# Kernel optimization log

Measured on AMD Instinct MI355X. Metric: run time of the kernel, lower is better.

The kernel has to match this reference:

```python
import jax, jax.numpy as jnp
import numpy as np

N = 100_000   # nodes
E = 1_600_000 # edges
C = 64        # in = hidden = out channels
H = 8         # heads
D = C // H    # head_dim = 8
R = 4         # relations
L = 2         # layers


def setup_inputs() -> dict:
    key = jax.random.key(0)
    ks = jax.random.split(key, 10)
    sc = 1.0 / np.sqrt(C)  # xavier-ish scale
    return {
        "x": jax.random.normal(ks[0], (N, C), jnp.float32),
        "edge_index": jax.random.randint(ks[1], (2, E), 0, N),
        "edge_type": jax.random.randint(ks[2], (E,), 0, R),
        "W_Q": jax.random.normal(ks[3], (L, R, H, C, D), jnp.float32) * sc,
        "W_K": jax.random.normal(ks[4], (L, R, H, C, D), jnp.float32) * sc,
        "W_V": jax.random.normal(ks[5], (L, R, H, C, D), jnp.float32) * sc,
        "W_concat": jax.random.normal(ks[6], (L, R, H * D, C), jnp.float32) * sc,
        "sem_w": jax.random.normal(ks[7], (L, C), jnp.float32) * sc,
        "sem_b": jnp.zeros((L,), jnp.float32),
        "W_self": jax.random.normal(ks[8], (L, C, C), jnp.float32) * sc,
        "ln_g": jnp.ones((L, C), jnp.float32),
        "ln_b": jnp.zeros((L, C), jnp.float32),
    }


def _layer(x, src, dst, edge_type, WQ, WK, WV, Wcat, sw, sb, Ws, g, b):
    inv_sqrt_d = 1.0 / np.sqrt(D)
    rel_msgs = []
    for r in range(R):  # small fixed relation loop
        mask = (edge_type == r).astype(x.dtype)             # (E,)
        Q = jnp.einsum('nc,hcd->nhd', x, WQ[r])             # (N,H,D)
        K = jnp.einsum('nc,hcd->nhd', x, WK[r])
        V = jnp.einsum('nc,hcd->nhd', x, WV[r])
        # edge-wise QK energy, leaky_relu(0.01), scatter-add into dst node
        energy = jnp.einsum('ehd,ehd->eh', Q[dst], K[src]) * inv_sqrt_d
        energy = jax.nn.leaky_relu(energy)                  # (E,H)
        alpha_n = jax.ops.segment_sum(energy * mask[:, None], dst,
                                      num_segments=N)       # (N,H)
        alpha = jax.nn.softmax(alpha_n, axis=0)             # softmax over nodes
        w = alpha[dst] * mask[:, None]                      # (E,H)
        m = jax.ops.segment_sum(w[:, :, None] * V[src], dst,
                                num_segments=N)             # (N,H,D)
        rel_msgs.append(m.reshape(N, H * D) @ Wcat[r])      # (N,C)
    stacked = jnp.stack(rel_msgs)                           # (R,N,C)
    beta = jax.nn.softmax(stacked @ sw + sb, axis=0)        # (R,N) semantic attn
    agg = jnp.einsum('rn,rnc->nc', beta, stacked)           # (N,C)
    y = x + jax.nn.gelu(x @ Ws + agg, approximate=False)
    mu = y.mean(-1, keepdims=True)
    var = y.var(-1, keepdims=True)
    return (y - mu) / jnp.sqrt(var + 1e-5) * g + b


def reference(x, edge_index, edge_type, W_Q, W_K, W_V, W_concat,
              sem_w, sem_b, W_self, ln_g, ln_b):
    src, dst = edge_index[0], edge_index[1]  # PyG source_to_target: j=row0, i=row1
    for l in range(L):
        x = _layer(x, src, dst, edge_type, W_Q[l], W_K[l], W_V[l], W_concat[l],
                   sem_w[l], sem_b[l], W_self[l], ln_g[l], ln_b[l])
        # inter-layer dropout omitted (inference / eval mode)
    return x
```

## Files before the change

### kernel.cpp

```cpp
#include <hip/hip_runtime.h>
#include <hip/hip_bf16.h>

#define NN 100000
#define EE 1600000
#define RRR 4
#define HHH 8
#define NT 400000
#define NBUCK 12500
#define BCAP 256

typedef unsigned int u32;
typedef unsigned short u16;
typedef unsigned long long u64;
typedef __attribute__((ext_vector_type(8))) short bf16x8;
typedef __attribute__((ext_vector_type(4))) float f32x4;

static constexpr size_t OFF_KV   = 0;
static constexpr size_t OFF_Q    = 25600000;
static constexpr size_t OFF_S    = 76800000;
static constexpr size_t OFF_AL   = 128000000;
static constexpr size_t OFF_PW   = 140800000;
static constexpr size_t OFF_PART = 141100000;
static constexpr size_t OFF_FIN  = 141110000;
static constexpr size_t OFF_BCNT = 141111008;
static constexpr size_t OFF_BST  = 141161008;
static constexpr size_t OFF_ROWP = 141211008;
static constexpr size_t OFF_EDG  = 142812012;

__device__ inline u16 f2bf(float f){
  union { __hip_bfloat16 h; u16 u; } cv; cv.h = __float2bfloat16(f); return cv.u;
}
__device__ inline float bf2f(u16 u){ return __uint_as_float(((u32)u) << 16); }

__global__ __launch_bounds__(256) void k_binit(u32* __restrict__ bcnt){
  int i = blockIdx.x * 256 + threadIdx.x;
  if (i < NBUCK) bcnt[i] = 0u;
}

__global__ __launch_bounds__(256) void k_bucket(const int* __restrict__ src, const int* __restrict__ dst,
                                                const int* __restrict__ typ, u32* __restrict__ bcnt,
                                                u64* __restrict__ bstore){
  for (int e = blockIdx.x * blockDim.x + threadIdx.x; e < EE; e += gridDim.x * blockDim.x){
    int seg = typ[e] * NN + dst[e];
    int b = seg >> 5;
    u32 pos = atomicAdd(&bcnt[b], 1u);
    if (pos < BCAP) bstore[(size_t)b * BCAP + pos] = ((u64)(u32)seg << 32) | (u32)src[e];
  }
}

__global__ __launch_bounds__(1024) void k_bscan(const u32* __restrict__ bcnt, u32* __restrict__ bstart,
                                                u32* __restrict__ rowp){
  __shared__ u32 tmp[1024];
  int t = threadIdx.x;
  const int PER = (NBUCK + 1023) / 1024;
  u32 loc[PER];
  u32 s = 0;
  #pragma unroll
  for (int i = 0; i < PER; i++){
    int idx = t * PER + i;
    u32 v = (idx < NBUCK) ? min(bcnt[idx], (u32)BCAP) : 0u;
    loc[i] = s; s += v;
  }
  tmp[t] = s; __syncthreads();
  for (int off = 1; off < 1024; off <<= 1){
    u32 add = (t >= off) ? tmp[t - off] : 0u; __syncthreads();
    tmp[t] += add; __syncthreads();
  }
  u32 base = tmp[t] - s;
  #pragma unroll
  for (int i = 0; i < PER; i++){
    int idx = t * PER + i;
    if (idx < NBUCK) bstart[idx] = base + loc[i];
  }
  if (t == 0) rowp[NT] = EE;
}

__global__ __launch_bounds__(256) void k_bsort(const u64* __restrict__ bstore, const u32* __restrict__ bcnt,
                                               const u32* __restrict__ bstart, u32* __restrict__ rowp,
                                               u32* __restrict__ edges){
  __shared__ u16 skey[BCAP];
  __shared__ u32 ssrc[BCAP];
  __shared__ u32 off[32], cur[32], excl[32];
  int b = blockIdx.x, t = threadIdx.x;
  u32 cnt = min(bcnt[b], (u32)BCAP);
  u32 base = bstart[b];
  if (t < 32) off[t] = 0u;
  __syncthreads();
  for (u32 i = t; i < cnt; i += 256){
    u64 v = bstore[(size_t)b * BCAP + i];
    skey[i] = (u16)((v >> 32) & 31u);
    ssrc[i] = (u32)v;
    atomicAdd(&off[(v >> 32) & 31u], 1u);
  }
  __syncthreads();
  if (t == 0){
    u32 acc = 0;
    #pragma unroll
    for (int k = 0; k < 32; k++){ u32 c = off[k]; excl[k] = acc; cur[k] = acc; acc += c; }
  }
  __syncthreads();
  if (t < 32){
    int seg = b * 32 + t;
    if (seg < NT) rowp[seg] = base + excl[t];
  }
  __syncthreads();
  for (u32 i = t; i < cnt; i += 256){
    u32 p = atomicAdd(&cur[skey[i]], 1u);
    edges[base + p] = ssrc[i];
  }
}

__global__ __launch_bounds__(256) void k_repackbf(const float* __restrict__ WQ, const float* __restrict__ WK,
                                                  const float* __restrict__ WV, const float* __restrict__ Wcat,
                                                  const float* __restrict__ Wself, u16* __restrict__ pwB){
  int t = blockIdx.x * 256 + threadIdx.x;
  if (t >= 2 * 17 * 4096) return;
  int l = t / (17 * 4096), rem = t % (17 * 4096);
  int mat = rem >> 12, idx = rem & 4095;
  int out = idx >> 6, c = idx & 63;
  float v;
  if (mat < 12){
    int kind = mat >> 2, r = mat & 3;
    int h = out >> 3, d = out & 7;
    const float* Wsrc = (kind == 0) ? WQ : (kind == 1) ? WK : WV;
    v = Wsrc[((((l * RRR + r) * HHH + h) * 64) + c) * 8 + d];
  } else if (mat == 12){
    v = Wself[(l * 64 + c) * 64 + out];
  } else {
    int r = mat - 13;
    v = Wcat[(((l * RRR + r) * 64) + c) * 64 + out];
  }
  pwB[t] = f2bf(v);
}


__global__ __launch_bounds__(256) void k_qkv(const float* __restrict__ x,
                                             const u16* __restrict__ pwQ, const u16* __restrict__ pwK,
                                             const u16* __restrict__ pwV,
                                             u16* __restrict__ Qr, u32* __restrict__ kvp){
  __shared__ u16 xa[64][72];
  __shared__ u16 wt[3][64][72];
  int t = threadIdx.x;
  int n0 = blockIdx.x * 64;
  {
    int row = t >> 2, c0 = (t & 3) * 16;
    int n = n0 + row;
    float4 v0 = {}, v1 = {}, v2 = {}, v3 = {};
    if (n < NN){
      const float4* xp = (const float4*)(x + (size_t)n * 64 + c0);
      v0 = xp[0]; v1 = xp[1]; v2 = xp[2]; v3 = xp[3];
    }
    ushort4* dp = (ushort4*)&xa[row][c0];
    dp[0] = make_ushort4(f2bf(v0.x), f2bf(v0.y), f2bf(v0.z), f2bf(v0.w));
    dp[1] = make_ushort4(f2bf(v1.x), f2bf(v1.y), f2bf(v1.z), f2bf(v1.w));
    dp[2] = make_ushort4(f2bf(v2.x), f2bf(v2.y), f2bf(v2.z), f2bf(v2.w));
    dp[3] = make_ushort4(f2bf(v3.x), f2bf(v3.y), f2bf(v3.z), f2bf(v3.w));
  }
  {
    const u32* p0 = (const u32*)pwQ;
    const u32* p1 = (const u32*)pwK;
    const u32* p2 = (const u32*)pwV;
    for (int idx = t; idx < 3 * 2048; idx += 256){
      int m = idx >> 11, rem = idx & 2047;
      int out = rem >> 5, cc = rem & 31;
      u32 w = (m == 0) ? p0[rem] : (m == 1) ? p1[rem] : p2[rem];
      *(u32*)&wt[m][out][cc * 2] = w;
    }
  }
  __syncthreads();
  int w = t >> 6, lane = t & 63;
  int ra = w * 16 + (lane & 15);
  int kg = (lane >> 4) * 8;
  int cb = lane & 15;
  int rb = (lane >> 4) * 4;
  bf16x8 a0 = *(const bf16x8*)&xa[ra][kg];
  bf16x8 a1 = *(const bf16x8*)&xa[ra][32 + kg];
  f32x4 z = {0.f, 0.f, 0.f, 0.f};
  {
    f32x4 acc[4] = {z, z, z, z};
    #pragma unroll
    for (int t4 = 0; t4 < 4; t4++){
      bf16x8 b0 = *(const bf16x8*)&wt[0][t4 * 16 + cb][kg];
      bf16x8 b1 = *(const bf16x8*)&wt[0][t4 * 16 + cb][32 + kg];
      acc[t4] = __builtin_amdgcn_mfma_f32_16x16x32_bf16(a0, b0, acc[t4], 0, 0, 0);
      acc[t4] = __builtin_amdgcn_mfma_f32_16x16x32_bf16(a1, b1, acc[t4], 0, 0, 0);
    }
    #pragma unroll
    for (int t4 = 0; t4 < 4; t4++){
      #pragma unroll
      for (int i = 0; i < 4; i++){
        int n = n0 + w * 16 + rb + i;
        if (n < NN) Qr[(size_t)n * 64 + t4 * 16 + cb] = f2bf(acc[t4][i]);
      }
    }
  }
  {
    f32x4 ak[4] = {z, z, z, z};
    f32x4 av[4] = {z, z, z, z};
    #pragma unroll
    for (int t4 = 0; t4 < 4; t4++){
      bf16x8 bk0 = *(const bf16x8*)&wt[1][t4 * 16 + cb][kg];
      bf16x8 bk1 = *(const bf16x8*)&wt[1][t4 * 16 + cb][32 + kg];
      bf16x8 bv0 = *(const bf16x8*)&wt[2][t4 * 16 + cb][kg];
      bf16x8 bv1 = *(const bf16x8*)&wt[2][t4 * 16 + cb][32 + kg];
      ak[t4] = __builtin_amdgcn_mfma_f32_16x16x32_bf16(a0, bk0, ak[t4], 0, 0, 0);
      ak[t4] = __builtin_amdgcn_mfma_f32_16x16x32_bf16(a1, bk1, ak[t4], 0, 0, 0);
      av[t4] = __builtin_amdgcn_mfma_f32_16x16x32_bf16(a0, bv0, av[t4], 0, 0, 0);
      av[t4] = __builtin_amdgcn_mfma_f32_16x16x32_bf16(a1, bv1, av[t4], 0, 0, 0);
    }
    #pragma unroll
    for (int t4 = 0; t4 < 4; t4++){
      #pragma unroll
      for (int i = 0; i < 4; i++){
        int n = n0 + w * 16 + rb + i;
        if (n < NN) kvp[(size_t)n * 64 + t4 * 16 + cb] = (u32)f2bf(ak[t4][i]) | ((u32)f2bf(av[t4][i]) << 16);
      }
    }
  }
}

__global__ __launch_bounds__(256) void k_self(const float* __restrict__ x, const u16* __restrict__ pwS,
                                              u16* __restrict__ outb){
  __shared__ u16 xa[64][72];
  __shared__ u16 wt[64][72];
  int t = threadIdx.x;
  int n0 = blockIdx.x * 64;
  {
    int row = t >> 2, c0 = (t & 3) * 16;
    int n = n0 + row;
    float4 v0 = {}, v1 = {}, v2 = {}, v3 = {};
    if (n < NN){
      const float4* xp = (const float4*)(x + (size_t)n * 64 + c0);
      v0 = xp[0]; v1 = xp[1]; v2 = xp[2]; v3 = xp[3];
    }
    ushort4* dp = (ushort4*)&xa[row][c0];
    dp[0] = make_ushort4(f2bf(v0.x), f2bf(v0.y), f2bf(v0.z), f2bf(v0.w));
    dp[1] = make_ushort4(f2bf(v1.x), f2bf(v1.y), f2bf(v1.z), f2bf(v1.w));
    dp[2] = make_ushort4(f2bf(v2.x), f2bf(v2.y), f2bf(v2.z), f2bf(v2.w));
    dp[3] = make_ushort4(f2bf(v3.x), f2bf(v3.y), f2bf(v3.z), f2bf(v3.w));
  }
  {
    const u32* p0 = (const u32*)pwS;
    for (int idx = t; idx < 2048; idx += 256){
      int out = idx >> 5, cc = idx & 31;
      *(u32*)&wt[out][cc * 2] = p0[idx];
    }
  }
  __syncthreads();
  int w = t >> 6, lane = t & 63;
  int ra = w * 16 + (lane & 15);
  int kg = (lane >> 4) * 8;
  int cb = lane & 15;
  int rb = (lane >> 4) * 4;
  bf16x8 a0 = *(const bf16x8*)&xa[ra][kg];
  bf16x8 a1 = *(const bf16x8*)&xa[ra][32 + kg];
  f32x4 z = {0.f, 0.f, 0.f, 0.f};
  f32x4 acc[4] = {z, z, z, z};
  #pragma unroll
  for (int t4 = 0; t4 < 4; t4++){
    bf16x8 b0 = *(const bf16x8*)&wt[t4 * 16 + cb][kg];
    bf16x8 b1 = *(const bf16x8*)&wt[t4 * 16 + cb][32 + kg];
    acc[t4] = __builtin_amdgcn_mfma_f32_16x16x32_bf16(a0, b0, acc[t4], 0, 0, 0);
    acc[t4] = __builtin_amdgcn_mfma_f32_16x16x32_bf16(a1, b1, acc[t4], 0, 0, 0);
  }
  #pragma unroll
  for (int t4 = 0; t4 < 4; t4++){
    #pragma unroll
    for (int i = 0; i < 4; i++){
      int n = n0 + w * 16 + rb + i;
      if (n < NN) outb[(size_t)n * 64 + t4 * 16 + cb] = f2bf(acc[t4][i]);
    }
  }
}

__global__ __launch_bounds__(256) void k_gather(const u32* __restrict__ edges, const u32* __restrict__ rowpR,
                                                const u32* __restrict__ kvp, const u16* __restrict__ Qr,
                                                u16* __restrict__ Sr, float* __restrict__ alphaR){
  int wid = threadIdx.x >> 6, lane = threadIdx.x & 63;
  int n = blockIdx.x * 4 + wid;
  float q = bf2f(Qr[(size_t)n * 64 + lane]);
  u32 beg = rowpR[n], end = rowpR[n + 1];
  float sa = 0.f, aa = 0.f;
  const float inv_sqrt_d = 0.35355339059327373f;
  for (u32 base = beg; base < end; base += 64){
    u32 cnt = (end - base < 64u) ? (end - base) : 64u;
    u32 eidx = (base + (u32)lane < end) ? edges[base + lane] : 0u;
    u32 j = 0;
    for (; j + 4 <= cnt; j += 4){
      int s0 = __shfl((int)eidx, (int)j);
      int s1 = __shfl((int)eidx, (int)j + 1);
      int s2 = __shfl((int)eidx, (int)j + 2);
      int s3 = __shfl((int)eidx, (int)j + 3);
      u32 w0 = kvp[(size_t)s0 * 64 + lane];
      u32 w1 = kvp[(size_t)s1 * 64 + lane];
      u32 w2 = kvp[(size_t)s2 * 64 + lane];
      u32 w3 = kvp[(size_t)s3 * 64 + lane];
      float p0 = q * bf2f((u16)(w0 & 0xFFFFu));
      float p1 = q * bf2f((u16)(w1 & 0xFFFFu));
      float p2 = q * bf2f((u16)(w2 & 0xFFFFu));
      float p3 = q * bf2f((u16)(w3 & 0xFFFFu));
      p0 += __shfl_xor(p0, 1); p1 += __shfl_xor(p1, 1); p2 += __shfl_xor(p2, 1); p3 += __shfl_xor(p3, 1);
      p0 += __shfl_xor(p0, 2); p1 += __shfl_xor(p1, 2); p2 += __shfl_xor(p2, 2); p3 += __shfl_xor(p3, 2);
      p0 += __shfl_xor(p0, 4); p1 += __shfl_xor(p1, 4); p2 += __shfl_xor(p2, 4); p3 += __shfl_xor(p3, 4);
      float e0 = p0 * inv_sqrt_d; e0 = (e0 > 0.f) ? e0 : 0.01f * e0;
      float e1 = p1 * inv_sqrt_d; e1 = (e1 > 0.f) ? e1 : 0.01f * e1;
      float e2 = p2 * inv_sqrt_d; e2 = (e2 > 0.f) ? e2 : 0.01f * e2;
      float e3 = p3 * inv_sqrt_d; e3 = (e3 > 0.f) ? e3 : 0.01f * e3;
      aa += (e0 + e1) + (e2 + e3);
      sa += (bf2f((u16)(w0 >> 16)) + bf2f((u16)(w1 >> 16))) +
            (bf2f((u16)(w2 >> 16)) + bf2f((u16)(w3 >> 16)));
    }
    for (; j < cnt; ++j){
      int s = __shfl((int)eidx, (int)j);
      u32 w = kvp[(size_t)s * 64 + lane];
      float p = q * bf2f((u16)(w & 0xFFFFu));
      p += __shfl_xor(p, 1);
      p += __shfl_xor(p, 2);
      p += __shfl_xor(p, 4);
      float e = p * inv_sqrt_d;
      e = (e > 0.f) ? e : 0.01f * e;
      aa += e;
      sa += bf2f((u16)(w >> 16));
    }
  }
  Sr[(size_t)n * 64 + lane] = f2bf(sa);
  if ((lane & 7) == 0) alphaR[(size_t)n * 8 + (lane >> 3)] = aa;
}

__global__ __launch_bounds__(256) void k_stats1(const float* __restrict__ alpha, float2* __restrict__ part){
  int col = blockIdx.x;
  int r = col >> 3, h = col & 7;
  int chunk = blockIdx.y;
  const int per = (NN + 31) / 32;
  int nbeg = chunk * per;
  int nend = nbeg + per; if (nend > NN) nend = NN;
  int t = threadIdx.x;
  float m = -1e30f, s = 0.f;
  for (int n = nbeg + t; n < nend; n += 256){
    float a = alpha[((size_t)r * NN + n) * 8 + h];
    if (a > m){ s *= expf(m - a); m = a; }
    s += expf(a - m);
  }
  __shared__ float sm[256], ss[256];
  sm[t] = m; ss[t] = s; __syncthreads();
  for (int off = 128; off > 0; off >>= 1){
    if (t < off){
      float m2 = sm[t + off], s2 = ss[t + off];
      float M = fmaxf(sm[t], m2);
      ss[t] = ss[t] * expf(sm[t] - M) + s2 * expf(m2 - M);
      sm[t] = M;
    }
    __syncthreads();
  }
  if (t == 0) part[col * 32 + chunk] = make_float2(sm[0], ss[0]);
}

__global__ void k_stats2(const float2* __restrict__ part, float2* __restrict__ fin){
  int col = threadIdx.x;
  if (col < 32){
    float M = -1e30f, S = 0.f;
    for (int i = 0; i < 32; i++){
      float2 p = part[col * 32 + i];
      float Mn = fmaxf(M, p.x);
      S = S * expf(M - Mn) + p.y * expf(p.x - Mn);
      M = Mn;
    }
    fin[col] = make_float2(M, 1.f / S);
  }
}

__global__ __launch_bounds__(256) void k_msg(const u16* __restrict__ S, const float* __restrict__ alpha,
                                             const float2* __restrict__ fin, const u16* __restrict__ pwCat,
                                             u16* __restrict__ stacked){
  __shared__ u16 xa[64][72];
  __shared__ u16 wt[64][72];
  int r = blockIdx.y;
  int t = threadIdx.x;
  int n0 = blockIdx.x * 64;
  {
    int row = t >> 2, c0 = (t & 3) * 16;
    int n = n0 + row;
    int na = (n < NN) ? n : (NN - 1);
    int h0 = c0 >> 3;
    float2 f0 = fin[r * 8 + h0];
    float2 f1 = fin[r * 8 + h0 + 1];
    float a0 = alpha[((size_t)r * NN + na) * 8 + h0];
    float a1 = alpha[((size_t)r * NN + na) * 8 + h0 + 1];
    float w0 = expf(a0 - f0.x) * f0.y;
    float w1 = expf(a1 - f1.x) * f1.y;
    const u32* sp = (const u32*)(S + ((size_t)r * NN + na) * 64 + c0);
    #pragma unroll
    for (int jj = 0; jj < 8; jj++){
      u32 bts = sp[jj];
      float wm = (jj < 4) ? w0 : w1;
      ushort2 o;
      o.x = f2bf(bf2f((u16)(bts & 0xFFFFu)) * wm);
      o.y = f2bf(bf2f((u16)(bts >> 16)) * wm);
      *(ushort2*)&xa[row][c0 + jj * 2] = o;
    }
  }
  {
    const u32* p0 = (const u32*)(pwCat + (size_t)r * 4096);
    for (int idx = t; idx < 2048; idx += 256){
      int out = idx >> 5, cc = idx & 31;
      *(u32*)&wt[out][cc * 2] = p0[idx];
    }
  }
  __syncthreads();
  int w = t >> 6, lane = t & 63;
  int ra = w * 16 + (lane & 15);
  int kg = (lane >> 4) * 8;
  int cb = lane & 15;
  int rb = (lane >> 4) * 4;
  bf16x8 a0 = *(const bf16x8*)&xa[ra][kg];
  bf16x8 a1 = *(const bf16x8*)&xa[ra][32 + kg];
  f32x4 z = {0.f, 0.f, 0.f, 0.f};
  f32x4 acc[4] = {z, z, z, z};
  #pragma unroll
  for (int t4 = 0; t4 < 4; t4++){
    bf16x8 b0 = *(const bf16x8*)&wt[t4 * 16 + cb][kg];
    bf16x8 b1 = *(const bf16x8*)&wt[t4 * 16 + cb][32 + kg];
    acc[t4] = __builtin_amdgcn_mfma_f32_16x16x32_bf16(a0, b0, acc[t4], 0, 0, 0);
    acc[t4] = __builtin_amdgcn_mfma_f32_16x16x32_bf16(a1, b1, acc[t4], 0, 0, 0);
  }
  #pragma unroll
  for (int t4 = 0; t4 < 4; t4++){
    #pragma unroll
    for (int i = 0; i < 4; i++){
      int n = n0 + w * 16 + rb + i;
      if (n < NN) stacked[((size_t)r * NN + n) * 64 + t4 * 16 + cb] = f2bf(acc[t4][i]);
    }
  }
}

__global__ __launch_bounds__(256) void k_final(const u16* __restrict__ stacked, const u16* __restrict__ selfb,
                                               const float* __restrict__ xin,
                                               const float* __restrict__ semw, const float* __restrict__ semb,
                                               const float* __restrict__ lng, const float* __restrict__ lnb,
                                               float* __restrict__ xout){
  int t = threadIdx.x;
  int wid = t >> 6, lane = t & 63;
  int n = blockIdx.x * 4 + wid;
  float st[4];
  #pragma unroll
  for (int r = 0; r < 4; r++) st[r] = bf2f(stacked[((size_t)r * NN + n) * 64 + lane]);
  float sw = semw[lane];
  float lg[4];
  #pragma unroll
  for (int r = 0; r < 4; r++){
    float p = st[r] * sw;
    #pragma unroll
    for (int o = 1; o < 64; o <<= 1) p += __shfl_xor(p, o);
    lg[r] = p + semb[0];
  }
  float mx = fmaxf(fmaxf(lg[0], lg[1]), fmaxf(lg[2], lg[3]));
  float e0 = expf(lg[0] - mx), e1 = expf(lg[1] - mx), e2 = expf(lg[2] - mx), e3 = expf(lg[3] - mx);
  float inv = 1.f / (e0 + e1 + e2 + e3);
  float agg = (e0 * st[0] + e1 * st[1] + e2 * st[2] + e3 * st[3]) * inv;
  float pre = bf2f(selfb[(size_t)n * 64 + lane]) + agg;
  float ge = 0.5f * pre * (1.f + erff(pre * 0.70710678118654752f));
  float y = xin[(size_t)n * 64 + lane] + ge;
  float mu = y;
  #pragma unroll
  for (int o = 1; o < 64; o <<= 1) mu += __shfl_xor(mu, o);
  mu *= (1.f / 64.f);
  float d = y - mu;
  float vv = d * d;
  #pragma unroll
  for (int o = 1; o < 64; o <<= 1) vv += __shfl_xor(vv, o);
  vv *= (1.f / 64.f);
  xout[(size_t)n * 64 + lane] = d * rsqrtf(vv + 1e-5f) * lng[lane] + lnb[lane];
}

extern "C" void kernel_launch(void* const* d_in, const int* in_sizes, int n_in,
                              void* d_out, int out_size, void* d_ws, size_t ws_size,
                              hipStream_t stream){
  const float* x0    = (const float*)d_in[0];
  const int*   eidx  = (const int*)d_in[1];
  const int*   etyp  = (const int*)d_in[2];
  const float* WQ    = (const float*)d_in[3];
  const float* WK    = (const float*)d_in[4];
  const float* WV    = (const float*)d_in[5];
  const float* Wcat  = (const float*)d_in[6];
  const float* semw  = (const float*)d_in[7];
  const float* semb  = (const float*)d_in[8];
  const float* Wself = (const float*)d_in[9];
  const float* lng   = (const float*)d_in[10];
  const float* lnb   = (const float*)d_in[11];
  float* out = (float*)d_out;
  char* ws = (char*)d_ws;

  const int* srcArr = eidx;
  const int* dstArr = eidx + EE;

  u32*  kvp      = (u32*)(ws + OFF_KV);
  u16*  selfb    = (u16*)(ws + OFF_KV);
  u16*  Qb       = (u16*)(ws + OFF_Q);
  u16*  stackedB = (u16*)(ws + OFF_Q);
  u16*  Sb       = (u16*)(ws + OFF_S);
  u64*  bstore   = (u64*)(ws + OFF_S);
  float* alphaB  = (float*)(ws + OFF_AL);
  u16*  pwB      = (u16*)(ws + OFF_PW);
  float2* part   = (float2*)(ws + OFF_PART);
  float2* fin    = (float2*)(ws + OFF_FIN);
  u32* bcnt   = (u32*)(ws + OFF_BCNT);
  u32* bstart = (u32*)(ws + OFF_BST);
  u32* rowp   = (u32*)(ws + OFF_ROWP);
  u32* edges  = (u32*)(ws + OFF_EDG);

  k_binit<<<(NBUCK + 255) / 256, 256, 0, stream>>>(bcnt);
  k_bucket<<<1024, 256, 0, stream>>>(srcArr, dstArr, etyp, bcnt, bstore);
  k_bscan<<<1, 1024, 0, stream>>>(bcnt, bstart, rowp);
  k_bsort<<<NBUCK, 256, 0, stream>>>(bstore, bcnt, bstart, rowp, edges);
  k_repackbf<<<(2 * 17 * 4096 + 255) / 256, 256, 0, stream>>>(WQ, WK, WV, Wcat, Wself, pwB);

  for (int l = 0; l < 2; l++){
    const float* xcur = (l == 0) ? x0 : out;
    const u16* pwL = pwB + (size_t)l * 17 * 4096;
    for (int r = 0; r < 4; r++){
      k_qkv<<<1563, 256, 0, stream>>>(xcur, pwL + (size_t)r * 4096, pwL + (size_t)(4 + r) * 4096,
                                      pwL + (size_t)(8 + r) * 4096, Qb + (size_t)r * NN * 64, kvp);
      k_gather<<<NN / 4, 256, 0, stream>>>(edges, rowp + (size_t)r * NN, kvp,
                                           Qb + (size_t)r * NN * 64,
                                           Sb + (size_t)r * NN * 64,
                                           alphaB + (size_t)r * NN * 8);
    }
    k_self<<<1563, 256, 0, stream>>>(xcur, pwL + (size_t)12 * 4096, selfb);
    k_stats1<<<dim3(32, 32), 256, 0, stream>>>(alphaB, part);
    k_stats2<<<1, 64, 0, stream>>>(part, fin);
    k_msg<<<dim3(1563, 4), 256, 0, stream>>>(Sb, alphaB, fin, pwL + (size_t)13 * 4096, stackedB);
    k_final<<<NN / 4, 256, 0, stream>>>(stackedB, selfb, xcur,
                                        semw + l * 64, semb + l, lng + l * 64, lnb + l * 64, out);
  }
  (void)in_sizes; (void)n_in; (void)out_size; (void)ws_size;
}
```

Before: 749.7 us.

## Replace atomic bucket CSR build with two-level histogram counting sort

```diff
diff --git a/kernel.cpp b/kernel.cpp
--- a/kernel.cpp
+++ b/kernel.cpp
@@ -6,12 +6,14 @@
 #define RRR 4
 #define HHH 8
 #define NT 400000
-#define NBUCK 12500
-#define BCAP 256
+#define GG 782
+#define SHIFT 9
+#define NBLK 512
+#define CHUNK 3125
+#define BMAX 2560
 
 typedef unsigned int u32;
 typedef unsigned short u16;
-typedef unsigned long long u64;
 typedef __attribute__((ext_vector_type(8))) short bf16x8;
 typedef __attribute__((ext_vector_type(4))) float f32x4;
 
@@ -22,91 +24,111 @@
 static constexpr size_t OFF_PW   = 140800000;
 static constexpr size_t OFF_PART = 141100000;
 static constexpr size_t OFF_FIN  = 141110000;
-static constexpr size_t OFF_BCNT = 141111008;
-static constexpr size_t OFF_BST  = 141161008;
-static constexpr size_t OFF_ROWP = 141211008;
-static constexpr size_t OFF_EDG  = 142812012;
+static constexpr size_t OFF_ROWP = 141365504;
+static constexpr size_t OFF_EDG  = 142965512;
+static constexpr size_t OFF_BSTORE = OFF_S;
+static constexpr size_t OFF_HIST   = OFF_S + 8000000;
+static constexpr size_t OFF_OFFA   = OFF_S + 16000000;
+static constexpr size_t OFF_BASE   = OFF_S + 24000000;
 
 __device__ inline u16 f2bf(float f){
   union { __hip_bfloat16 h; u16 u; } cv; cv.h = __float2bfloat16(f); return cv.u;
 }
 __device__ inline float bf2f(u16 u){ return __uint_as_float(((u32)u) << 16); }
 
-__global__ __launch_bounds__(256) void k_binit(u32* __restrict__ bcnt){
-  int i = blockIdx.x * 256 + threadIdx.x;
-  if (i < NBUCK) bcnt[i] = 0u;
-}
-
-__global__ __launch_bounds__(256) void k_bucket(const int* __restrict__ src, const int* __restrict__ dst,
-                                                const int* __restrict__ typ, u32* __restrict__ bcnt,
-                                                u64* __restrict__ bstore){
-  for (int e = blockIdx.x * blockDim.x + threadIdx.x; e < EE; e += gridDim.x * blockDim.x){
+__global__ __launch_bounds__(256) void k_histA(const int* __restrict__ dst, const int* __restrict__ typ,
+                                               u32* __restrict__ Hist){
+  __shared__ u32 h[GG];
+  int b = blockIdx.x, t = threadIdx.x;
+  for (int g = t; g < GG; g += 256) h[g] = 0u;
+  __syncthreads();
+  int e0 = b * CHUNK;
+  for (int e = e0 + t; e < e0 + CHUNK; e += 256){
     int seg = typ[e] * NN + dst[e];
-    int b = seg >> 5;
-    u32 pos = atomicAdd(&bcnt[b], 1u);
-    if (pos < BCAP) bstore[(size_t)b * BCAP + pos] = ((u64)(u32)seg << 32) | (u32)src[e];
-  }
-}
-
-__global__ __launch_bounds__(1024) void k_bscan(const u32* __restrict__ bcnt, u32* __restrict__ bstart,
-                                                u32* __restrict__ rowp){
-  __shared__ u32 tmp[1024];
+    atomicAdd(&h[seg >> SHIFT], 1u);
+  }
+  __syncthreads();
+  for (int g = t; g < GG; g += 256) Hist[(size_t)b * GG + g] = h[g];
+}
+
+__global__ __launch_bounds__(1024) void k_base(const u32* __restrict__ Hist, u32* __restrict__ Base,
+                                               u32* __restrict__ rowp){
+  __shared__ u32 tot[GG];
   int t = threadIdx.x;
-  const int PER = (NBUCK + 1023) / 1024;
-  u32 loc[PER];
-  u32 s = 0;
-  #pragma unroll
-  for (int i = 0; i < PER; i++){
-    int idx = t * PER + i;
-    u32 v = (idx < NBUCK) ? min(bcnt[idx], (u32)BCAP) : 0u;
-    loc[i] = s; s += v;
-  }
-  tmp[t] = s; __syncthreads();
-  for (int off = 1; off < 1024; off <<= 1){
-    u32 add = (t >= off) ? tmp[t - off] : 0u; __syncthreads();
-    tmp[t] += add; __syncthreads();
-  }
-  u32 base = tmp[t] - s;
-  #pragma unroll
-  for (int i = 0; i < PER; i++){
-    int idx = t * PER + i;
-    if (idx < NBUCK) bstart[idx] = base + loc[i];
-  }
-  if (t == 0) rowp[NT] = EE;
-}
-
-__global__ __launch_bounds__(256) void k_bsort(const u64* __restrict__ bstore, const u32* __restrict__ bcnt,
-                                               const u32* __restrict__ bstart, u32* __restrict__ rowp,
-                                               u32* __restrict__ edges){
-  __shared__ u16 skey[BCAP];
-  __shared__ u32 ssrc[BCAP];
-  __shared__ u32 off[32], cur[32], excl[32];
-  int b = blockIdx.x, t = threadIdx.x;
-  u32 cnt = min(bcnt[b], (u32)BCAP);
-  u32 base = bstart[b];
-  if (t < 32) off[t] = 0u;
-  __syncthreads();
-  for (u32 i = t; i < cnt; i += 256){
-    u64 v = bstore[(size_t)b * BCAP + i];
-    skey[i] = (u16)((v >> 32) & 31u);
-    ssrc[i] = (u32)v;
-    atomicAdd(&off[(v >> 32) & 31u], 1u);
+  if (t < GG){
+    u32 s = 0;
+    for (int b = 0; b < NBLK; b++) s += Hist[(size_t)b * GG + t];
+    tot[t] = s;
   }
   __syncthreads();
   if (t == 0){
     u32 acc = 0;
-    #pragma unroll
-    for (int k = 0; k < 32; k++){ u32 c = off[k]; excl[k] = acc; cur[k] = acc; acc += c; }
-  }
-  __syncthreads();
-  if (t < 32){
-    int seg = b * 32 + t;
-    if (seg < NT) rowp[seg] = base + excl[t];
-  }
+    for (int g = 0; g < GG; g++){ u32 c = tot[g]; Base[g] = acc; acc += c; }
+    Base[GG] = acc;
+    rowp[NT] = EE;
+  }
+}
+
+__global__ __launch_bounds__(512) void k_off(const u32* __restrict__ Hist, const u32* __restrict__ Base,
+                                             u32* __restrict__ Off){
+  __shared__ u32 v[NBLK];
+  int g = blockIdx.x, t = threadIdx.x;
+  v[t] = Hist[(size_t)t * GG + g];
+  __syncthreads();
+  if (t == 0){
+    u32 acc = Base[g];
+    for (int b = 0; b < NBLK; b++){ u32 c = v[b]; v[b] = acc; acc += c; }
+  }
+  __syncthreads();
+  Off[(size_t)g * NBLK + t] = v[t];
+}
+
+__global__ __launch_bounds__(256) void k_fill(const int* __restrict__ src, const int* __restrict__ dst,
+                                              const int* __restrict__ typ, const u32* __restrict__ Off,
+                                              u32* __restrict__ bstore){
+  __shared__ u32 cur[GG];
+  int b = blockIdx.x, t = threadIdx.x;
+  for (int g = t; g < GG; g += 256) cur[g] = Off[(size_t)g * NBLK + b];
+  __syncthreads();
+  int e0 = b * CHUNK;
+  for (int e = e0 + t; e < e0 + CHUNK; e += 256){
+    int seg = typ[e] * NN + dst[e];
+    u32 pos = atomicAdd(&cur[seg >> SHIFT], 1u);
+    bstore[pos] = ((u32)(seg & 511) << 17) | (u32)src[e];
+  }
+}
+
+__global__ __launch_bounds__(256) void k_sortD(const u32* __restrict__ bstore, const u32* __restrict__ Base,
+                                               u32* __restrict__ rowp, u32* __restrict__ edges){
+  __shared__ u32 ent[BMAX];
+  __shared__ u32 binc[512], bexc[512];
+  int g = blockIdx.x, t = threadIdx.x;
+  u32 base = Base[g];
+  u32 cnt = Base[g + 1] - base;
+  if (cnt > (u32)BMAX) cnt = (u32)BMAX;
+  for (int i = t; i < 512; i += 256) binc[i] = 0u;
   __syncthreads();
   for (u32 i = t; i < cnt; i += 256){
-    u32 p = atomicAdd(&cur[skey[i]], 1u);
-    edges[base + p] = ssrc[i];
+    u32 v = bstore[base + i];
+    ent[i] = v;
+    atomicAdd(&binc[v >> 17], 1u);
+  }
+  __syncthreads();
+  if (t == 0){
+    u32 acc = 0;
+    #pragma unroll 8
+    for (int s = 0; s < 512; s++){ u32 c = binc[s]; bexc[s] = acc; binc[s] = acc; acc += c; }
+  }
+  __syncthreads();
+  for (int s = t; s < 512; s += 256){
+    int seg = g * 512 + s;
+    if (seg < NT) rowp[seg] = base + bexc[s];
+  }
+  __syncthreads();
+  for (u32 i = t; i < cnt; i += 256){
+    u32 v = ent[i];
+    u32 p = atomicAdd(&binc[v >> 17], 1u);
+    edges[base + p] = v & 0x1FFFFu;
   }
 }
 
@@ -498,20 +520,22 @@
   u16*  Qb       = (u16*)(ws + OFF_Q);
   u16*  stackedB = (u16*)(ws + OFF_Q);
   u16*  Sb       = (u16*)(ws + OFF_S);
-  u64*  bstore   = (u64*)(ws + OFF_S);
   float* alphaB  = (float*)(ws + OFF_AL);
   u16*  pwB      = (u16*)(ws + OFF_PW);
   float2* part   = (float2*)(ws + OFF_PART);
   float2* fin    = (float2*)(ws + OFF_FIN);
-  u32* bcnt   = (u32*)(ws + OFF_BCNT);
-  u32* bstart = (u32*)(ws + OFF_BST);
   u32* rowp   = (u32*)(ws + OFF_ROWP);
   u32* edges  = (u32*)(ws + OFF_EDG);
-
-  k_binit<<<(NBUCK + 255) / 256, 256, 0, stream>>>(bcnt);
-  k_bucket<<<1024, 256, 0, stream>>>(srcArr, dstArr, etyp, bcnt, bstore);
-  k_bscan<<<1, 1024, 0, stream>>>(bcnt, bstart, rowp);
-  k_bsort<<<NBUCK, 256, 0, stream>>>(bstore, bcnt, bstart, rowp, edges);
+  u32* bstore = (u32*)(ws + OFF_BSTORE);
+  u32* Hist   = (u32*)(ws + OFF_HIST);
+  u32* Off    = (u32*)(ws + OFF_OFFA);
+  u32* Base   = (u32*)(ws + OFF_BASE);
+
+  k_histA<<<NBLK, 256, 0, stream>>>(dstArr, etyp, Hist);
+  k_base<<<1, 1024, 0, stream>>>(Hist, Base, rowp);
+  k_off<<<GG, 512, 0, stream>>>(Hist, Base, Off);
+  k_fill<<<NBLK, 256, 0, stream>>>(srcArr, dstArr, etyp, Off, bstore);
+  k_sortD<<<GG, 256, 0, stream>>>(bstore, Base, rowp, edges);
   k_repackbf<<<(2 * 17 * 4096 + 255) / 256, 256, 0, stream>>>(WQ, WK, WV, Wcat, Wself, pwB);
 
   for (int l = 0; l < 2; l++){
```

Measured after the change: 710.7 us. -5.2%, faster.
